# Kernel tuning notes

Hardware: AMD Instinct MI355X
Metric: run time of the kernel (lower is better)

## Reference

```python
import jax, jax.numpy as jnp
import numpy as np

P = 16; H_IMG = 384; W_IMG = 384; D = 1024
N_LAYERS = 24; DI = 2048; DS = 16; DTR = 64; DC = 4; EPS = 1e-5


def setup_inputs() -> dict:
    key = jax.random.key(0)
    ks = jax.random.split(key, 12)
    B = 2
    inp = {}
    inp["x"] = jax.random.normal(ks[0], (B, 3, H_IMG, W_IMG), jnp.float32)
    inp["patch_w"] = jax.random.normal(ks[1], (D, 3, P, P), jnp.float32) * 0.02
    inp["patch_b"] = jnp.zeros((D,), jnp.float32)
    inp["pos_embed"] = jax.random.normal(ks[2], (1, (H_IMG // P) * (W_IMG // P), D), jnp.float32) * 0.02
    inp["ln_g"] = jnp.ones((N_LAYERS, D), jnp.float32)
    inp["ln_b"] = jnp.zeros((N_LAYERS, D), jnp.float32)
    inp["in_w"] = jax.random.normal(ks[3], (N_LAYERS, 2 * DI, D), jnp.float32) * 0.02
    inp["conv_w"] = jax.random.normal(ks[4], (N_LAYERS, DI, DC), jnp.float32) * 0.1
    inp["conv_b"] = jnp.zeros((N_LAYERS, DI), jnp.float32)
    inp["xproj_w"] = jax.random.normal(ks[5], (N_LAYERS, DTR + 2 * DS, DI), jnp.float32) * 0.02
    inp["dt_w"] = jax.random.normal(ks[6], (N_LAYERS, DI, DTR), jnp.float32) * 0.02
    inp["dt_b"] = jnp.full((N_LAYERS, DI), -4.0, jnp.float32)  # softplus(-4) ~ 0.018
    inp["A_log"] = jnp.broadcast_to(jnp.log(jnp.arange(1, DS + 1, dtype=jnp.float32)), (N_LAYERS, DI, DS)).copy()
    inp["D_param"] = jnp.ones((N_LAYERS, DI), jnp.float32)
    inp["out_w"] = jax.random.normal(ks[7], (N_LAYERS, D, DI), jnp.float32) * 0.02
    return inp


def _layer_norm(x, g, b):
    mu = jnp.mean(x, axis=-1, keepdims=True)
    var = jnp.var(x, axis=-1, keepdims=True)
    return (x - mu) * jax.lax.rsqrt(var + EPS) * g + b


def _mamba_block(x, p):
    g, bn, Win, Wc, bc, Wxp, Wdt, bdt, Alog, Dd, Wout = p
    u = _layer_norm(x, g, bn)                          # [B,L,D]
    xz = jnp.einsum('bld,ed->ble', u, Win)             # [B,L,2*DI]
    xi, z = jnp.split(xz, 2, axis=-1)
    # causal depthwise conv1d along L (kernel DC=4)
    xt = jnp.moveaxis(xi, 1, 2)                        # [B,DI,L]
    L = xt.shape[-1]
    xpad = jnp.pad(xt, ((0, 0), (0, 0), (DC - 1, 0)))
    xc = sum(Wc[:, k][None, :, None] * xpad[:, :, k:k + L] for k in range(DC)) + bc[None, :, None]
    xc = jax.nn.silu(jnp.moveaxis(xc, 1, 2))           # [B,L,DI]
    dbc = jnp.einsum('bld,ed->ble', xc, Wxp)           # [B,L,DTR+2*DS]
    dt, Bm, Cm = jnp.split(dbc, [DTR, DTR + DS], axis=-1)
    dt = jax.nn.softplus(jnp.einsum('blr,dr->bld', dt, Wdt) + bdt)  # [B,L,DI]
    A = -jnp.exp(Alog)                                 # [DI,DS]
    dA = jnp.exp(dt[..., None] * A)                    # [B,L,DI,DS]
    dBx = (dt * xc)[..., None] * Bm[:, :, None, :]     # [B,L,DI,DS]

    def step(h, inp):
        dA_t, dBx_t, C_t = inp
        h = dA_t * h + dBx_t                           # [B,DI,DS]
        y = jnp.einsum('bds,bs->bd', h, C_t)
        return h, y

    h0 = jnp.zeros((x.shape[0], DI, DS), x.dtype)
    xs = (jnp.moveaxis(dA, 1, 0), jnp.moveaxis(dBx, 1, 0), jnp.moveaxis(Cm, 1, 0))
    _, ys = jax.lax.scan(step, h0, xs)                 # ys: [L,B,DI]
    y = jnp.moveaxis(ys, 0, 1) + Dd * xc
    y = y * jax.nn.silu(z)
    return x + jnp.einsum('ble,de->bld', y, Wout)


def _forward(x, patch_w, patch_b, pos_embed, ln_g, ln_b, in_w, conv_w, conv_b,
             xproj_w, dt_w, dt_b, A_log, D_param, out_w):
    feat = jax.lax.conv_general_dilated(
        x, patch_w, (P, P), 'VALID',
        dimension_numbers=('NCHW', 'OIHW', 'NCHW')) + patch_b[None, :, None, None]
    Bn, Dd, Hh, Ww = feat.shape
    tok = feat.reshape(Bn, Dd, Hh * Ww).transpose(0, 2, 1)  # [B,L,D]
    h0, w0 = H_IMG // P, W_IMG // P
    pe = pos_embed.reshape(1, h0, w0, Dd)
    pe = jax.image.resize(pe, (1, Hh, Ww, Dd), 'bilinear')  # align_corners=False
    tok = tok + pe.reshape(1, Hh * Ww, Dd)
    params = (ln_g, ln_b, in_w, conv_w, conv_b, xproj_w, dt_w, dt_b, A_log, D_param, out_w)

    def layer(carry, p):
        return jax.checkpoint(_mamba_block)(carry, p), None

    tok, _ = jax.lax.scan(layer, tok, params)
    return tok


def reference(x, patch_w, patch_b, pos_embed, ln_g, ln_b, in_w, conv_w, conv_b,
              xproj_w, dt_w, dt_b, A_log, D_param, out_w):
    return _forward(x, patch_w, patch_b, pos_embed, ln_g, ln_b, in_w, conv_w, conv_b,
                    xproj_w, dt_w, dt_b, A_log, D_param, out_w)
```

## Files before the change

### kernel.cpp

```cpp
#include <hip/hip_runtime.h>
#include <hip/hip_bf16.h>
#include <math.h>

#define PATCH   16
#define HIMG    384
#define WIMG    384
#define DMODEL  1024
#define NLAYERS 24
#define DI      2048
#define DSTATE  16
#define DTR     64
#define DC      4
#define LN_EPS  1e-5f
#define BATCH   2
#define GRIDTOK 24
#define LTOK    (GRIDTOK*GRIDTOK)
#define NTOK    (BATCH*LTOK)
#define KPATCH  (3*PATCH*PATCH)
#define NCH     16
#define LC      (LTOK/NCH)

typedef __attribute__((ext_vector_type(8))) short short8;
typedef __attribute__((ext_vector_type(4))) float f32x4;

__device__ __forceinline__ float sigmoidf_(float v) { return 1.f / (1.f + __expf(-v)); }
__device__ __forceinline__ unsigned short f2bf(float f) {
    __hip_bfloat16 h = __float2bfloat16(f);
    return *(unsigned short*)&h;
}

__global__ void im2col_kernel(const float* __restrict__ x, float* __restrict__ xcol) {
    int idx = blockIdx.x * blockDim.x + threadIdx.x;
    if (idx >= NTOK * KPATCH) return;
    int t = idx / KPATCH, k = idx % KPATCH;
    int b = t / LTOK, hw = t % LTOK;
    int h = hw / GRIDTOK, w = hw % GRIDTOK;
    int c = k / (PATCH*PATCH), r = k % (PATCH*PATCH);
    int i = r / PATCH, j = r % PATCH;
    xcol[idx] = x[(((size_t)(b*3 + c)*HIMG) + h*PATCH + i)*WIMG + w*PATCH + j];
}

__global__ __launch_bounds__(256) void layernorm_kernel(
        const float* __restrict__ x, const float* __restrict__ g,
        const float* __restrict__ b, unsigned short* __restrict__ u) {
    const int t = blockIdx.x;
    const int tid = threadIdx.x;
    const float4 xv = ((const float4*)(x + (size_t)t * DMODEL))[tid];
    float s = xv.x + xv.y + xv.z + xv.w;
    float q = xv.x*xv.x + xv.y*xv.y + xv.z*xv.z + xv.w*xv.w;
    #pragma unroll
    for (int off = 32; off >= 1; off >>= 1) {
        s += __shfl_xor(s, off);
        q += __shfl_xor(q, off);
    }
    __shared__ float red[8];
    if ((tid & 63) == 0) { red[tid >> 6] = s; red[4 + (tid >> 6)] = q; }
    __syncthreads();
    s = red[0] + red[1] + red[2] + red[3];
    q = red[4] + red[5] + red[6] + red[7];
    const float mu   = s * (1.f / DMODEL);
    const float var  = q * (1.f / DMODEL) - mu * mu;
    const float rstd = rsqrtf(var + LN_EPS);
    const float4 gv = ((const float4*)g)[tid];
    const float4 bv = ((const float4*)b)[tid];
    ushort4 o;
    o.x = f2bf((xv.x - mu) * rstd * gv.x + bv.x);
    o.y = f2bf((xv.y - mu) * rstd * gv.y + bv.y);
    o.z = f2bf((xv.z - mu) * rstd * gv.z + bv.z);
    o.w = f2bf((xv.w - mu) * rstd * gv.w + bv.w);
    ((ushort4*)(u + (size_t)t * DMODEL))[tid] = o;
}

template<int SPLITK>
__global__ __launch_bounds__(256) void gemm_mfma_bt(
        const unsigned short* __restrict__ A, int lda,
        const float* __restrict__ B, int ldb,
        float* __restrict__ C, int M, int N, int Ksub) {
    __shared__ unsigned short As[128 * 64];
    __shared__ unsigned short Bs[128 * 64];
    const int tid = threadIdx.x;
    const int m0 = blockIdx.x * 128;
    const int n0 = blockIdx.y * 128;
    const int koff = SPLITK ? blockIdx.z * Ksub : 0;
    if (SPLITK) C += (size_t)blockIdx.z * M * N;

    const int lane = tid & 63;
    const int wid  = tid >> 6;
    const int wm = (wid >> 1) * 64;
    const int wn = (wid & 1) * 64;
    const int fr = lane & 15;
    const int cb = lane >> 4;

    const int srow = tid >> 3;
    const int skc  = tid & 7;

    f32x4 acc[4][4];
    #pragma unroll
    for (int i = 0; i < 4; ++i)
        #pragma unroll
        for (int j = 0; j < 4; ++j) acc[i][j] = (f32x4){0.f, 0.f, 0.f, 0.f};

    uint4  areg[4];
    float4 breg[4][2];

    const int nk = Ksub / 64;
    #pragma unroll
    for (int i = 0; i < 4; ++i) {
        const int r = srow + 32 * i;
        areg[i] = *(const uint4*)(A + (size_t)(m0 + r) * lda + koff + skc * 8);
        const float* bp = B + (size_t)(n0 + r) * ldb + koff + skc * 8;
        breg[i][0] = *(const float4*)bp;
        breg[i][1] = *(const float4*)(bp + 4);
    }

    for (int ks = 0; ks < nk; ++ks) {
        __syncthreads();
        #pragma unroll
        for (int i = 0; i < 4; ++i) {
            const int r = srow + 32 * i;
            const int idx = r * 64 + ((skc ^ (r & 7)) << 3);
            *(uint4*)&As[idx] = areg[i];
            const float* bf = (const float*)&breg[i][0];
            short8 hv;
            #pragma unroll
            for (int j = 0; j < 8; ++j) hv[j] = (short)f2bf(bf[j]);
            *(short8*)&Bs[idx] = hv;
        }
        __syncthreads();
        if (ks + 1 < nk) {
            const int k1 = koff + (ks + 1) * 64;
            #pragma unroll
            for (int i = 0; i < 4; ++i) {
                const int r = srow + 32 * i;
                areg[i] = *(const uint4*)(A + (size_t)(m0 + r) * lda + k1 + skc * 8);
                const float* bp = B + (size_t)(n0 + r) * ldb + k1 + skc * 8;
                breg[i][0] = *(const float4*)bp;
                breg[i][1] = *(const float4*)(bp + 4);
            }
        }
        #pragma unroll
        for (int kk = 0; kk < 2; ++kk) {
            short8 af[4], bfr[4];
            #pragma unroll
            for (int mi = 0; mi < 4; ++mi) {
                const int row = wm + mi * 16 + fr;
                af[mi] = *(const short8*)&As[row * 64 + (((kk * 4 + cb) ^ (row & 7)) << 3)];
            }
            #pragma unroll
            for (int ni = 0; ni < 4; ++ni) {
                const int row = wn + ni * 16 + fr;
                bfr[ni] = *(const short8*)&Bs[row * 64 + (((kk * 4 + cb) ^ (row & 7)) << 3)];
            }
            #pragma unroll
            for (int mi = 0; mi < 4; ++mi)
                #pragma unroll
                for (int ni = 0; ni < 4; ++ni)
                    acc[mi][ni] = __builtin_amdgcn_mfma_f32_16x16x32_bf16(
                        af[mi], bfr[ni], acc[mi][ni], 0, 0, 0);
        }
    }

    #pragma unroll
    for (int mi = 0; mi < 4; ++mi) {
        const int rbase = m0 + wm + mi * 16 + cb * 4;
        #pragma unroll
        for (int ni = 0; ni < 4; ++ni) {
            const int col = n0 + wn + ni * 16 + fr;
            #pragma unroll
            for (int j = 0; j < 4; ++j)
                C[(size_t)(rbase + j) * N + col] = acc[mi][ni][j];
        }
    }
}

__global__ void reduce4_resadd_kernel(const float* __restrict__ part,
                                      float* __restrict__ tok, int n4) {
    int i = blockIdx.x * blockDim.x + threadIdx.x;
    if (i >= n4) return;
    float4 v = ((const float4*)part)[i];
    const float4 p1 = ((const float4*)part)[(size_t)1 * n4 + i];
    const float4 p2 = ((const float4*)part)[(size_t)2 * n4 + i];
    const float4 p3 = ((const float4*)part)[(size_t)3 * n4 + i];
    float4 t = ((float4*)tok)[i];
    t.x += v.x + p1.x + p2.x + p3.x;
    t.y += v.y + p1.y + p2.y + p3.y;
    t.z += v.z + p1.z + p2.z + p3.z;
    t.w += v.w + p1.w + p2.w + p3.w;
    ((float4*)tok)[i] = t;
}

enum { E_NONE = 0, E_BIAS_POS = 1, E_BIAS_SOFTPLUS = 2 };

template<int EPI>
__global__ __launch_bounds__(256) void gemm_nt(
        const float* __restrict__ A, int lda,
        const float* __restrict__ B, int ldb,
        float* __restrict__ C, int M, int N, int Ksub,
        const float* __restrict__ bias, const float* __restrict__ aux) {
    __shared__ float As[16][64];
    __shared__ float Bs[16][64];
    const int tid = threadIdx.x;
    const int m0 = blockIdx.x * 64;
    const int n0 = blockIdx.y * 64;
    const int koff = blockIdx.z * Ksub;
    C += (size_t)blockIdx.z * M * N;

    const int lrow = tid >> 2;
    const int kq   = tid & 3;
    const float* aptr = A + (size_t)(m0 + lrow) * lda + koff + kq * 4;
    const bool   bok  = (n0 + lrow) < N;
    const float* bptr = B + (size_t)(n0 + lrow) * ldb + koff + kq * 4;

    float acc[4][4] = {{0.f}};
    for (int k0 = 0; k0 < Ksub; k0 += 16) {
        const float4 av = *(const float4*)(aptr + k0);
        const float4 bv = bok ? *(const float4*)(bptr + k0) : make_float4(0.f, 0.f, 0.f, 0.f);
        __syncthreads();
        As[kq*4+0][lrow] = av.x; As[kq*4+1][lrow] = av.y;
        As[kq*4+2][lrow] = av.z; As[kq*4+3][lrow] = av.w;
        Bs[kq*4+0][lrow] = bv.x; Bs[kq*4+1][lrow] = bv.y;
        Bs[kq*4+2][lrow] = bv.z; Bs[kq*4+3][lrow] = bv.w;
        __syncthreads();
        #pragma unroll
        for (int kk = 0; kk < 16; ++kk) {
            const float4 a = *(const float4*)&As[kk][(tid >> 4) << 2];
            const float4 b = *(const float4*)&Bs[kk][(tid & 15) << 2];
            const float aa[4] = {a.x, a.y, a.z, a.w};
            const float bb[4] = {b.x, b.y, b.z, b.w};
            #pragma unroll
            for (int i = 0; i < 4; ++i)
                #pragma unroll
                for (int j = 0; j < 4; ++j)
                    acc[i][j] = fmaf(aa[i], bb[j], acc[i][j]);
        }
    }

    const int mb = m0 + ((tid >> 4) << 2);
    const int nb = n0 + ((tid & 15) << 2);
    if (nb >= N) return;
    #pragma unroll
    for (int i = 0; i < 4; ++i) {
        const int m = mb + i;
        float4 v = make_float4(acc[i][0], acc[i][1], acc[i][2], acc[i][3]);
        float* cp = C + (size_t)m * N + nb;
        if (EPI == E_BIAS_POS) {
            const float4 bz = *(const float4*)(bias + nb);
            const float4 pz = *(const float4*)(aux + (size_t)(m % LTOK) * DMODEL + nb);
            v.x += bz.x + pz.x; v.y += bz.y + pz.y; v.z += bz.z + pz.z; v.w += bz.w + pz.w;
        } else if (EPI == E_BIAS_SOFTPLUS) {
            const float4 bz = *(const float4*)(bias + nb);
            v.x += bz.x; v.y += bz.y; v.z += bz.z; v.w += bz.w;
            v.x = (v.x > 20.f) ? v.x : log1pf(__expf(v.x));
            v.y = (v.y > 20.f) ? v.y : log1pf(__expf(v.y));
            v.z = (v.z > 20.f) ? v.z : log1pf(__expf(v.z));
            v.w = (v.w > 20.f) ? v.w : log1pf(__expf(v.w));
        }
        *(float4*)cp = v;
    }
}

__global__ void conv1d_silu_kernel(const float* __restrict__ xz,
                                   const float* __restrict__ wc,
                                   const float* __restrict__ bc,
                                   float* __restrict__ xc) {
    int idx = blockIdx.x * blockDim.x + threadIdx.x;
    if (idx >= NTOK * DI) return;
    const int t = idx >> 11;
    const int e = idx & (DI - 1);
    const int l = t % LTOK;
    const float4 w = *(const float4*)(wc + e * DC);
    const float* xp = xz + (size_t)t * (2*DI) + e;
    float acc = bc[e] + w.w * xp[0];
    if (l >= 1) acc += w.z * xp[-(2*DI)];
    if (l >= 2) acc += w.y * xp[-2*(2*DI)];
    if (l >= 3) acc += w.x * xp[-3*(2*DI)];
    xc[idx] = acc * sigmoidf_(acc);
}

__global__ __launch_bounds__(256) void scan_pass1(
        const float* __restrict__ dt, const float* __restrict__ xc,
        const float* __restrict__ dbc, const float* __restrict__ Alog,
        float* __restrict__ Fst, float* __restrict__ sdt) {
    const int tid = threadIdx.x;
    const int e  = blockIdx.x * 256 + tid;
    const int c  = blockIdx.y;
    const int b  = blockIdx.z;
    const int l0 = c * LC;
    const size_t tb = (size_t)b * LTOK + l0;

    __shared__ float Bs[LC][16];
    for (int idx = tid; idx < LC * 16; idx += 256) {
        const int row = idx >> 4, s = idx & 15;
        Bs[row][s] = dbc[(tb + row) * 96 + 64 + s];
    }

    float Aval[DSTATE];
    {
        const float* ap = Alog + (size_t)e * DSTATE;
        #pragma unroll
        for (int s = 0; s < DSTATE; ++s) Aval[s] = -__expf(ap[s]);
    }
    __syncthreads();

    const float* dtp = dt + tb * DI + e;
    const float* xcp = xc + tb * DI + e;
    float h[DSTATE];
    #pragma unroll
    for (int s = 0; s < DSTATE; ++s) h[s] = 0.f;
    float sum_dt = 0.f;

    float dtv = dtp[0], xcv = xcp[0];
    for (int l = 0; l < LC; ++l) {
        float dtn = 0.f, xcn = 0.f;
        if (l + 1 < LC) { dtn = dtp[(size_t)(l+1) * DI]; xcn = xcp[(size_t)(l+1) * DI]; }
        sum_dt += dtv;
        const float dx = dtv * xcv;
        const float4* brow = (const float4*)&Bs[l][0];
        const float4 b0 = brow[0], b1 = brow[1], b2 = brow[2], b3 = brow[3];
        const float bb[16] = {b0.x,b0.y,b0.z,b0.w, b1.x,b1.y,b1.z,b1.w,
                              b2.x,b2.y,b2.z,b2.w, b3.x,b3.y,b3.z,b3.w};
        #pragma unroll
        for (int s = 0; s < DSTATE; ++s)
            h[s] = fmaf(__expf(dtv * Aval[s]), h[s], dx * bb[s]);
        dtv = dtn; xcv = xcn;
    }

    float4* Fp = (float4*)(Fst + ((((size_t)b * NCH + c) * DI) + e) * DSTATE);
    #pragma unroll
    for (int q = 0; q < 4; ++q)
        Fp[q] = make_float4(h[q*4+0], h[q*4+1], h[q*4+2], h[q*4+3]);
    sdt[((size_t)b * NCH + c) * DI + e] = sum_dt;
}

__global__ __launch_bounds__(256) void scan_pass2(
        const float* __restrict__ Fst, const float* __restrict__ sdt,
        const float* __restrict__ Alog, float* __restrict__ Hst) {
    const int idx = blockIdx.x * 256 + threadIdx.x;
    const int s = idx & 15;
    const int e = (idx >> 4) & (DI - 1);
    const int b = idx >> 15;
    const float Aval = -__expf(Alog[(size_t)e * DSTATE + s]);
    float h = 0.f;
    for (int c = 0; c < NCH; ++c) {
        const size_t base = ((size_t)b * NCH + c) * DI + e;
        Hst[base * DSTATE + s] = h;
        h = fmaf(__expf(Aval * sdt[base]), h, Fst[base * DSTATE + s]);
    }
}

__global__ __launch_bounds__(256) void scan_pass3(
        const float* __restrict__ dt, const float* __restrict__ xc,
        const float* __restrict__ dbc, const float* __restrict__ xz,
        const float* __restrict__ Alog, const float* __restrict__ Dp,
        const float* __restrict__ Hst, unsigned short* __restrict__ y) {
    const int tid = threadIdx.x;
    const int e  = blockIdx.x * 256 + tid;
    const int c  = blockIdx.y;
    const int b  = blockIdx.z;
    const int l0 = c * LC;
    const size_t tb = (size_t)b * LTOK + l0;

    __shared__ float BCs[LC][32];
    for (int idx = tid; idx < LC * 32; idx += 256) {
        const int row = idx >> 5, col = idx & 31;
        BCs[row][col] = dbc[(tb + row) * 96 + 64 + col];
    }

    float Aval[DSTATE];
    {
        const float* ap = Alog + (size_t)e * DSTATE;
        #pragma unroll
        for (int s = 0; s < DSTATE; ++s) Aval[s] = -__expf(ap[s]);
    }
    const float Dv = Dp[e];

    float h[DSTATE];
    {
        const float4* Hp = (const float4*)(Hst + ((((size_t)b * NCH + c) * DI) + e) * DSTATE);
        #pragma unroll
        for (int q = 0; q < 4; ++q) {
            const float4 hv = Hp[q];
            h[q*4+0] = hv.x; h[q*4+1] = hv.y; h[q*4+2] = hv.z; h[q*4+3] = hv.w;
        }
    }
    __syncthreads();

    const float* dtp = dt + tb * DI + e;
    const float* xcp = xc + tb * DI + e;
    const float* zp  = xz + tb * (2*DI) + DI + e;
    unsigned short* yp = y + tb * DI + e;

    float dtv = dtp[0], xcv = xcp[0], zv = zp[0];
    for (int l = 0; l < LC; ++l) {
        float dtn = 0.f, xcn = 0.f, zn = 0.f;
        if (l + 1 < LC) {
            dtn = dtp[(size_t)(l+1) * DI];
            xcn = xcp[(size_t)(l+1) * DI];
            zn  = zp[(size_t)(l+1) * (2*DI)];
        }
        const float dx = dtv * xcv;
        const float4* brow = (const float4*)&BCs[l][0];
        const float4 b0 = brow[0], b1 = brow[1], b2 = brow[2], b3 = brow[3];
        const float4 c0 = brow[4], c1 = brow[5], c2 = brow[6], c3 = brow[7];
        const float bb[16] = {b0.x,b0.y,b0.z,b0.w, b1.x,b1.y,b1.z,b1.w,
                              b2.x,b2.y,b2.z,b2.w, b3.x,b3.y,b3.z,b3.w};
        const float cc[16] = {c0.x,c0.y,c0.z,c0.w, c1.x,c1.y,c1.z,c1.w,
                              c2.x,c2.y,c2.z,c2.w, c3.x,c3.y,c3.z,c3.w};
        float yv = 0.f;
        #pragma unroll
        for (int s = 0; s < DSTATE; ++s) {
            h[s] = fmaf(__expf(dtv * Aval[s]), h[s], dx * bb[s]);
            yv = fmaf(h[s], cc[s], yv);
        }
        yp[(size_t)l * DI] = f2bf((yv + Dv * xcv) * (zv * sigmoidf_(zv)));
        dtv = dtn; xcv = xcn; zv = zn;
    }
}

__global__ void reduce8_kernel(const float* __restrict__ part, float* __restrict__ out, int n) {
    int i = blockIdx.x * blockDim.x + threadIdx.x;
    if (i >= n) return;
    float s = 0.f;
    #pragma unroll
    for (int z = 0; z < 8; ++z) s += part[(size_t)z * n + i];
    out[i] = s;
}

extern "C" void kernel_launch(void* const* d_in, const int* in_sizes, int n_in,
                              void* d_out, int out_size, void* d_ws, size_t ws_size,
                              hipStream_t stream) {
    const float* x       = (const float*)d_in[0];
    const float* patch_w = (const float*)d_in[1];
    const float* patch_b = (const float*)d_in[2];
    const float* pos     = (const float*)d_in[3];
    const float* ln_g    = (const float*)d_in[4];
    const float* ln_b    = (const float*)d_in[5];
    const float* in_w    = (const float*)d_in[6];
    const float* conv_w  = (const float*)d_in[7];
    const float* conv_b  = (const float*)d_in[8];
    const float* xproj_w = (const float*)d_in[9];
    const float* dt_w    = (const float*)d_in[10];
    const float* dt_b    = (const float*)d_in[11];
    const float* A_log   = (const float*)d_in[12];
    const float* D_par   = (const float*)d_in[13];
    const float* out_w   = (const float*)d_in[14];

    float* tok = (float*)d_out;
    float* ws  = (float*)d_ws;
    float* Xcol = ws;  ws += (size_t)NTOK * KPATCH;
    unsigned short* u_bf = (unsigned short*)ws; ws += (size_t)NTOK * DMODEL / 2;
    float* xz   = ws;  ws += (size_t)NTOK * 2 * DI;
    float* xc   = ws;  ws += (size_t)NTOK * DI;
    float* dbcP = ws;  ws += (size_t)8 * NTOK * 96;
    float* dbc  = ws;  ws += (size_t)NTOK * 96;
    float* dtb  = ws;  ws += (size_t)NTOK * DI;
    unsigned short* yb_bf = (unsigned short*)ws; ws += (size_t)NTOK * DI / 2;
    float* Fst  = ws;  ws += (size_t)BATCH * NCH * DI * DSTATE;
    float* Hst  = ws;  ws += (size_t)BATCH * NCH * DI * DSTATE;
    float* sdt  = ws;  ws += (size_t)BATCH * NCH * DI;

    im2col_kernel<<<(NTOK*KPATCH + 255)/256, 256, 0, stream>>>(x, Xcol);
    gemm_nt<E_BIAS_POS><<<dim3(NTOK/64, DMODEL/64), 256, 0, stream>>>(
        Xcol, KPATCH, patch_w, KPATCH, tok, NTOK, DMODEL, KPATCH, patch_b, pos);

    for (int layer = 0; layer < NLAYERS; ++layer) {
        const float* Wg  = ln_g    + (size_t)layer * DMODEL;
        const float* Wb  = ln_b    + (size_t)layer * DMODEL;
        const float* Win = in_w    + (size_t)layer * 2 * DI * DMODEL;
        const float* Wc  = conv_w  + (size_t)layer * DI * DC;
        const float* Bc  = conv_b  + (size_t)layer * DI;
        const float* Wxp = xproj_w + (size_t)layer * 96 * DI;
        const float* Wdt = dt_w    + (size_t)layer * DI * DTR;
        const float* Bdt = dt_b    + (size_t)layer * DI;
        const float* Al  = A_log   + (size_t)layer * DI * DSTATE;
        const float* Dd  = D_par   + (size_t)layer * DI;
        const float* Wo  = out_w   + (size_t)layer * DMODEL * DI;

        layernorm_kernel<<<NTOK, 256, 0, stream>>>(tok, Wg, Wb, u_bf);
        gemm_mfma_bt<0><<<dim3(NTOK/128, (2*DI)/128, 1), 256, 0, stream>>>(
            u_bf, DMODEL, Win, DMODEL, xz, NTOK, 2*DI, DMODEL);
        conv1d_silu_kernel<<<(NTOK*DI + 255)/256, 256, 0, stream>>>(xz, Wc, Bc, xc);
        gemm_nt<E_NONE><<<dim3(NTOK/64, 2, 8), 256, 0, stream>>>(
            xc, DI, Wxp, DI, dbcP, NTOK, 96, DI/8, nullptr, nullptr);
        reduce8_kernel<<<(NTOK*96 + 255)/256, 256, 0, stream>>>(dbcP, dbc, NTOK*96);
        gemm_nt<E_BIAS_SOFTPLUS><<<dim3(NTOK/64, DI/64), 256, 0, stream>>>(
            dbc, 96, Wdt, DTR, dtb, NTOK, DI, DTR, Bdt, nullptr);
        scan_pass1<<<dim3(DI/256, NCH, BATCH), 256, 0, stream>>>(
            dtb, xc, dbc, Al, Fst, sdt);
        scan_pass2<<<(BATCH*DI*DSTATE)/256, 256, 0, stream>>>(Fst, sdt, Al, Hst);
        scan_pass3<<<dim3(DI/256, NCH, BATCH), 256, 0, stream>>>(
            dtb, xc, dbc, xz, Al, Dd, Hst, yb_bf);
        gemm_mfma_bt<1><<<dim3(NTOK/128, DMODEL/128, 4), 256, 0, stream>>>(
            yb_bf, DI, Wo, DI, xz, NTOK, DMODEL, DI/4);
        reduce4_resadd_kernel<<<(NTOK*DMODEL/4 + 255)/256, 256, 0, stream>>>(
            xz, tok, NTOK*DMODEL/4);
    }
}
```

Measured before the change: 4.660 ms.

## Pre-convert weights to bf16, move small GEMMs to MFMA, fuse reduce with layernorm

Every weight matrix is converted to bf16 once at the start, so the MFMA GEMMs load bf16 B tiles directly instead of converting fp32 inside the inner loop. The patch embedding, x-projection and dt-projection GEMMs move from scalar fp32 FMA kernels to bf16 MFMA kernels, with a dedicated 96-column kernel for x-proj. The split-K residual reduce is fused with the next layer's layernorm. scan_pass2 is removed by having pass3 recompute the chunk prefix state itself. The weight conversion pass adds extra memory traffic per call, and the bf16 inputs to the small projections lower precision.

```diff
diff --git a/kernel.cpp b/kernel.cpp
--- a/kernel.cpp
+++ b/kernel.cpp
@@ -29,7 +29,16 @@
     return *(unsigned short*)&h;
 }
 
-__global__ void im2col_kernel(const float* __restrict__ x, float* __restrict__ xcol) {
+__global__ void f2bf_kernel(const float* __restrict__ in, unsigned short* __restrict__ out, int n4) {
+    for (int i = blockIdx.x * blockDim.x + threadIdx.x; i < n4; i += gridDim.x * blockDim.x) {
+        const float4 v = ((const float4*)in)[i];
+        ushort4 o;
+        o.x = f2bf(v.x); o.y = f2bf(v.y); o.z = f2bf(v.z); o.w = f2bf(v.w);
+        ((ushort4*)out)[i] = o;
+    }
+}
+
+__global__ void im2col_kernel(const float* __restrict__ x, unsigned short* __restrict__ xcol) {
     int idx = blockIdx.x * blockDim.x + threadIdx.x;
     if (idx >= NTOK * KPATCH) return;
     int t = idx / KPATCH, k = idx % KPATCH;
@@ -37,7 +46,7 @@
     int h = hw / GRIDTOK, w = hw % GRIDTOK;
     int c = k / (PATCH*PATCH), r = k % (PATCH*PATCH);
     int i = r / PATCH, j = r % PATCH;
-    xcol[idx] = x[(((size_t)(b*3 + c)*HIMG) + h*PATCH + i)*WIMG + w*PATCH + j];
+    xcol[idx] = f2bf(x[(((size_t)(b*3 + c)*HIMG) + h*PATCH + i)*WIMG + w*PATCH + j]);
 }
 
 __global__ __launch_bounds__(256) void layernorm_kernel(
@@ -71,11 +80,12 @@
     ((ushort4*)(u + (size_t)t * DMODEL))[tid] = o;
 }
 
-template<int SPLITK>
-__global__ __launch_bounds__(256) void gemm_mfma_bt(
+template<int SPLITK, int EPI>
+__global__ __launch_bounds__(256) void gemm_bb(
         const unsigned short* __restrict__ A, int lda,
-        const float* __restrict__ B, int ldb,
-        float* __restrict__ C, int M, int N, int Ksub) {
+        const unsigned short* __restrict__ B, int ldb,
+        float* __restrict__ C, int M, int N, int Ksub,
+        const float* __restrict__ bias, const float* __restrict__ aux) {
     __shared__ unsigned short As[128 * 64];
     __shared__ unsigned short Bs[128 * 64];
     const int tid = threadIdx.x;
@@ -100,17 +110,13 @@
         #pragma unroll
         for (int j = 0; j < 4; ++j) acc[i][j] = (f32x4){0.f, 0.f, 0.f, 0.f};
 
-    uint4  areg[4];
-    float4 breg[4][2];
-
+    uint4 areg[4], breg[4];
     const int nk = Ksub / 64;
     #pragma unroll
     for (int i = 0; i < 4; ++i) {
         const int r = srow + 32 * i;
         areg[i] = *(const uint4*)(A + (size_t)(m0 + r) * lda + koff + skc * 8);
-        const float* bp = B + (size_t)(n0 + r) * ldb + koff + skc * 8;
-        breg[i][0] = *(const float4*)bp;
-        breg[i][1] = *(const float4*)(bp + 4);
+        breg[i] = *(const uint4*)(B + (size_t)(n0 + r) * ldb + koff + skc * 8);
     }
 
     for (int ks = 0; ks < nk; ++ks) {
@@ -120,11 +126,7 @@
             const int r = srow + 32 * i;
             const int idx = r * 64 + ((skc ^ (r & 7)) << 3);
             *(uint4*)&As[idx] = areg[i];
-            const float* bf = (const float*)&breg[i][0];
-            short8 hv;
-            #pragma unroll
-            for (int j = 0; j < 8; ++j) hv[j] = (short)f2bf(bf[j]);
-            *(short8*)&Bs[idx] = hv;
+            *(uint4*)&Bs[idx] = breg[i];
         }
         __syncthreads();
         if (ks + 1 < nk) {
@@ -133,9 +135,7 @@
             for (int i = 0; i < 4; ++i) {
                 const int r = srow + 32 * i;
                 areg[i] = *(const uint4*)(A + (size_t)(m0 + r) * lda + k1 + skc * 8);
-                const float* bp = B + (size_t)(n0 + r) * ldb + k1 + skc * 8;
-                breg[i][0] = *(const float4*)bp;
-                breg[i][1] = *(const float4*)(bp + 4);
+                breg[i] = *(const uint4*)(B + (size_t)(n0 + r) * ldb + k1 + skc * 8);
             }
         }
         #pragma unroll
@@ -167,102 +167,133 @@
         for (int ni = 0; ni < 4; ++ni) {
             const int col = n0 + wn + ni * 16 + fr;
             #pragma unroll
+            for (int j = 0; j < 4; ++j) {
+                float v = acc[mi][ni][j];
+                if (EPI == 1) {
+                    v += bias[col];
+                    v = (v > 20.f) ? v : log1pf(__expf(v));
+                } else if (EPI == 2) {
+                    v += bias[col] + aux[(size_t)((rbase + j) % LTOK) * DMODEL + col];
+                }
+                C[(size_t)(rbase + j) * N + col] = v;
+            }
+        }
+    }
+}
+
+__global__ __launch_bounds__(256) void gemm_xproj(
+        const unsigned short* __restrict__ A,
+        const unsigned short* __restrict__ B,
+        float* __restrict__ C) {
+    __shared__ unsigned short As[128 * 64];
+    __shared__ unsigned short Bs[96 * 64];
+    const int tid = threadIdx.x;
+    const int m0 = blockIdx.x * 128;
+    const int koff = blockIdx.y * (DI / 8);
+    C += (size_t)blockIdx.y * NTOK * 96;
+
+    const int lane = tid & 63;
+    const int wid  = tid >> 6;
+    const int wm = wid * 32;
+    const int fr = lane & 15;
+    const int cb = lane >> 4;
+    const int srow = tid >> 3;
+    const int skc  = tid & 7;
+
+    f32x4 acc[2][6];
+    #pragma unroll
+    for (int i = 0; i < 2; ++i)
+        #pragma unroll
+        for (int j = 0; j < 6; ++j) acc[i][j] = (f32x4){0.f, 0.f, 0.f, 0.f};
+
+    uint4 areg[4], breg[3];
+    #pragma unroll
+    for (int i = 0; i < 4; ++i)
+        areg[i] = *(const uint4*)(A + (size_t)(m0 + srow + 32 * i) * DI + koff + skc * 8);
+    #pragma unroll
+    for (int i = 0; i < 3; ++i) {
+        const int idx = tid + 256 * i;
+        breg[i] = *(const uint4*)(B + (size_t)(idx >> 3) * DI + koff + (idx & 7) * 8);
+    }
+
+    const int nk = (DI / 8) / 64;
+    for (int ks = 0; ks < nk; ++ks) {
+        __syncthreads();
+        #pragma unroll
+        for (int i = 0; i < 4; ++i) {
+            const int r = srow + 32 * i;
+            *(uint4*)&As[r * 64 + ((skc ^ (r & 7)) << 3)] = areg[i];
+        }
+        #pragma unroll
+        for (int i = 0; i < 3; ++i) {
+            const int idx = tid + 256 * i;
+            const int r = idx >> 3, kc = idx & 7;
+            *(uint4*)&Bs[r * 64 + ((kc ^ (r & 7)) << 3)] = breg[i];
+        }
+        __syncthreads();
+        if (ks + 1 < nk) {
+            const int k1 = koff + (ks + 1) * 64;
+            #pragma unroll
+            for (int i = 0; i < 4; ++i)
+                areg[i] = *(const uint4*)(A + (size_t)(m0 + srow + 32 * i) * DI + k1 + skc * 8);
+            #pragma unroll
+            for (int i = 0; i < 3; ++i) {
+                const int idx = tid + 256 * i;
+                breg[i] = *(const uint4*)(B + (size_t)(idx >> 3) * DI + k1 + (idx & 7) * 8);
+            }
+        }
+        #pragma unroll
+        for (int kk = 0; kk < 2; ++kk) {
+            short8 af[2], bfr[6];
+            #pragma unroll
+            for (int mi = 0; mi < 2; ++mi) {
+                const int row = wm + mi * 16 + fr;
+                af[mi] = *(const short8*)&As[row * 64 + (((kk * 4 + cb) ^ (row & 7)) << 3)];
+            }
+            #pragma unroll
+            for (int ni = 0; ni < 6; ++ni) {
+                const int row = ni * 16 + fr;
+                bfr[ni] = *(const short8*)&Bs[row * 64 + (((kk * 4 + cb) ^ (row & 7)) << 3)];
+            }
+            #pragma unroll
+            for (int mi = 0; mi < 2; ++mi)
+                #pragma unroll
+                for (int ni = 0; ni < 6; ++ni)
+                    acc[mi][ni] = __builtin_amdgcn_mfma_f32_16x16x32_bf16(
+                        af[mi], bfr[ni], acc[mi][ni], 0, 0, 0);
+        }
+    }
+
+    #pragma unroll
+    for (int mi = 0; mi < 2; ++mi) {
+        const int rbase = m0 + wm + mi * 16 + cb * 4;
+        #pragma unroll
+        for (int ni = 0; ni < 6; ++ni) {
+            const int col = ni * 16 + fr;
+            #pragma unroll
             for (int j = 0; j < 4; ++j)
-                C[(size_t)(rbase + j) * N + col] = acc[mi][ni][j];
-        }
-    }
-}
-
-__global__ void reduce4_resadd_kernel(const float* __restrict__ part,
-                                      float* __restrict__ tok, int n4) {
+                C[(size_t)(rbase + j) * 96 + col] = acc[mi][ni][j];
+        }
+    }
+}
+
+__global__ void reduce8_kernel(const float* __restrict__ part, float* __restrict__ out,
+                               unsigned short* __restrict__ out64, int n) {
     int i = blockIdx.x * blockDim.x + threadIdx.x;
-    if (i >= n4) return;
-    float4 v = ((const float4*)part)[i];
-    const float4 p1 = ((const float4*)part)[(size_t)1 * n4 + i];
-    const float4 p2 = ((const float4*)part)[(size_t)2 * n4 + i];
-    const float4 p3 = ((const float4*)part)[(size_t)3 * n4 + i];
-    float4 t = ((float4*)tok)[i];
-    t.x += v.x + p1.x + p2.x + p3.x;
-    t.y += v.y + p1.y + p2.y + p3.y;
-    t.z += v.z + p1.z + p2.z + p3.z;
-    t.w += v.w + p1.w + p2.w + p3.w;
-    ((float4*)tok)[i] = t;
-}
-
-enum { E_NONE = 0, E_BIAS_POS = 1, E_BIAS_SOFTPLUS = 2 };
-
-template<int EPI>
-__global__ __launch_bounds__(256) void gemm_nt(
-        const float* __restrict__ A, int lda,
-        const float* __restrict__ B, int ldb,
-        float* __restrict__ C, int M, int N, int Ksub,
-        const float* __restrict__ bias, const float* __restrict__ aux) {
-    __shared__ float As[16][64];
-    __shared__ float Bs[16][64];
-    const int tid = threadIdx.x;
-    const int m0 = blockIdx.x * 64;
-    const int n0 = blockIdx.y * 64;
-    const int koff = blockIdx.z * Ksub;
-    C += (size_t)blockIdx.z * M * N;
-
-    const int lrow = tid >> 2;
-    const int kq   = tid & 3;
-    const float* aptr = A + (size_t)(m0 + lrow) * lda + koff + kq * 4;
-    const bool   bok  = (n0 + lrow) < N;
-    const float* bptr = B + (size_t)(n0 + lrow) * ldb + koff + kq * 4;
-
-    float acc[4][4] = {{0.f}};
-    for (int k0 = 0; k0 < Ksub; k0 += 16) {
-        const float4 av = *(const float4*)(aptr + k0);
-        const float4 bv = bok ? *(const float4*)(bptr + k0) : make_float4(0.f, 0.f, 0.f, 0.f);
-        __syncthreads();
-        As[kq*4+0][lrow] = av.x; As[kq*4+1][lrow] = av.y;
-        As[kq*4+2][lrow] = av.z; As[kq*4+3][lrow] = av.w;
-        Bs[kq*4+0][lrow] = bv.x; Bs[kq*4+1][lrow] = bv.y;
-        Bs[kq*4+2][lrow] = bv.z; Bs[kq*4+3][lrow] = bv.w;
-        __syncthreads();
-        #pragma unroll
-        for (int kk = 0; kk < 16; ++kk) {
-            const float4 a = *(const float4*)&As[kk][(tid >> 4) << 2];
-            const float4 b = *(const float4*)&Bs[kk][(tid & 15) << 2];
-            const float aa[4] = {a.x, a.y, a.z, a.w};
-            const float bb[4] = {b.x, b.y, b.z, b.w};
-            #pragma unroll
-            for (int i = 0; i < 4; ++i)
-                #pragma unroll
-                for (int j = 0; j < 4; ++j)
-                    acc[i][j] = fmaf(aa[i], bb[j], acc[i][j]);
-        }
-    }
-
-    const int mb = m0 + ((tid >> 4) << 2);
-    const int nb = n0 + ((tid & 15) << 2);
-    if (nb >= N) return;
-    #pragma unroll
-    for (int i = 0; i < 4; ++i) {
-        const int m = mb + i;
-        float4 v = make_float4(acc[i][0], acc[i][1], acc[i][2], acc[i][3]);
-        float* cp = C + (size_t)m * N + nb;
-        if (EPI == E_BIAS_POS) {
-            const float4 bz = *(const float4*)(bias + nb);
-            const float4 pz = *(const float4*)(aux + (size_t)(m % LTOK) * DMODEL + nb);
-            v.x += bz.x + pz.x; v.y += bz.y + pz.y; v.z += bz.z + pz.z; v.w += bz.w + pz.w;
-        } else if (EPI == E_BIAS_SOFTPLUS) {
-            const float4 bz = *(const float4*)(bias + nb);
-            v.x += bz.x; v.y += bz.y; v.z += bz.z; v.w += bz.w;
-            v.x = (v.x > 20.f) ? v.x : log1pf(__expf(v.x));
-            v.y = (v.y > 20.f) ? v.y : log1pf(__expf(v.y));
-            v.z = (v.z > 20.f) ? v.z : log1pf(__expf(v.z));
-            v.w = (v.w > 20.f) ? v.w : log1pf(__expf(v.w));
-        }
-        *(float4*)cp = v;
-    }
+    if (i >= n) return;
+    float s = 0.f;
+    #pragma unroll
+    for (int z = 0; z < 8; ++z) s += part[(size_t)z * n + i];
+    out[i] = s;
+    const int col = i % 96;
+    if (col < 64) out64[(i / 96) * 64 + col] = f2bf(s);
 }
 
 __global__ void conv1d_silu_kernel(const float* __restrict__ xz,
                                    const float* __restrict__ wc,
                                    const float* __restrict__ bc,
-                                   float* __restrict__ xc) {
+                                   float* __restrict__ xc,
+                                   unsigned short* __restrict__ xc_bf) {
     int idx = blockIdx.x * blockDim.x + threadIdx.x;
     if (idx >= NTOK * DI) return;
     const int t = idx >> 11;
@@ -274,7 +305,9 @@
     if (l >= 1) acc += w.z * xp[-(2*DI)];
     if (l >= 2) acc += w.y * xp[-2*(2*DI)];
     if (l >= 3) acc += w.x * xp[-3*(2*DI)];
-    xc[idx] = acc * sigmoidf_(acc);
+    const float r = acc * sigmoidf_(acc);
+    xc[idx] = r;
+    xc_bf[idx] = f2bf(r);
 }
 
 __global__ __launch_bounds__(256) void scan_pass1(
@@ -332,27 +365,12 @@
     sdt[((size_t)b * NCH + c) * DI + e] = sum_dt;
 }
 
-__global__ __launch_bounds__(256) void scan_pass2(
-        const float* __restrict__ Fst, const float* __restrict__ sdt,
-        const float* __restrict__ Alog, float* __restrict__ Hst) {
-    const int idx = blockIdx.x * 256 + threadIdx.x;
-    const int s = idx & 15;
-    const int e = (idx >> 4) & (DI - 1);
-    const int b = idx >> 15;
-    const float Aval = -__expf(Alog[(size_t)e * DSTATE + s]);
-    float h = 0.f;
-    for (int c = 0; c < NCH; ++c) {
-        const size_t base = ((size_t)b * NCH + c) * DI + e;
-        Hst[base * DSTATE + s] = h;
-        h = fmaf(__expf(Aval * sdt[base]), h, Fst[base * DSTATE + s]);
-    }
-}
-
 __global__ __launch_bounds__(256) void scan_pass3(
         const float* __restrict__ dt, const float* __restrict__ xc,
         const float* __restrict__ dbc, const float* __restrict__ xz,
         const float* __restrict__ Alog, const float* __restrict__ Dp,
-        const float* __restrict__ Hst, unsigned short* __restrict__ y) {
+        const float* __restrict__ Fst, const float* __restrict__ sdt,
+        unsigned short* __restrict__ y) {
     const int tid = threadIdx.x;
     const int e  = blockIdx.x * 256 + tid;
     const int c  = blockIdx.y;
@@ -375,13 +393,18 @@
     const float Dv = Dp[e];
 
     float h[DSTATE];
-    {
-        const float4* Hp = (const float4*)(Hst + ((((size_t)b * NCH + c) * DI) + e) * DSTATE);
-        #pragma unroll
-        for (int q = 0; q < 4; ++q) {
-            const float4 hv = Hp[q];
-            h[q*4+0] = hv.x; h[q*4+1] = hv.y; h[q*4+2] = hv.z; h[q*4+3] = hv.w;
-        }
+    #pragma unroll
+    for (int s = 0; s < DSTATE; ++s) h[s] = 0.f;
+    for (int c2 = 0; c2 < c; ++c2) {
+        const size_t base = ((size_t)b * NCH + c2) * DI + e;
+        const float sd = sdt[base];
+        const float4* Fp = (const float4*)(Fst + base * DSTATE);
+        const float4 f0 = Fp[0], f1 = Fp[1], f2 = Fp[2], f3 = Fp[3];
+        const float ff[16] = {f0.x,f0.y,f0.z,f0.w, f1.x,f1.y,f1.z,f1.w,
+                              f2.x,f2.y,f2.z,f2.w, f3.x,f3.y,f3.z,f3.w};
+        #pragma unroll
+        for (int s = 0; s < DSTATE; ++s)
+            h[s] = fmaf(__expf(Aval[s] * sd), h[s], ff[s]);
     }
     __syncthreads();
 
@@ -417,13 +440,50 @@
     }
 }
 
-__global__ void reduce8_kernel(const float* __restrict__ part, float* __restrict__ out, int n) {
-    int i = blockIdx.x * blockDim.x + threadIdx.x;
-    if (i >= n) return;
-    float s = 0.f;
-    #pragma unroll
-    for (int z = 0; z < 8; ++z) s += part[(size_t)z * n + i];
-    out[i] = s;
+template<bool DO_LN>
+__global__ __launch_bounds__(256) void reduce4_ln_kernel(
+        const float* __restrict__ part, float* __restrict__ tok,
+        const float* __restrict__ g, const float* __restrict__ b,
+        unsigned short* __restrict__ u) {
+    const int t = blockIdx.x;
+    const int tid = threadIdx.x;
+    const int n4 = NTOK * DMODEL / 4;
+    const int i = t * 256 + tid;
+    float4 v = ((const float4*)part)[i];
+    const float4 p1 = ((const float4*)part)[(size_t)1 * n4 + i];
+    const float4 p2 = ((const float4*)part)[(size_t)2 * n4 + i];
+    const float4 p3 = ((const float4*)part)[(size_t)3 * n4 + i];
+    float4 tv = ((float4*)tok)[i];
+    tv.x += v.x + p1.x + p2.x + p3.x;
+    tv.y += v.y + p1.y + p2.y + p3.y;
+    tv.z += v.z + p1.z + p2.z + p3.z;
+    tv.w += v.w + p1.w + p2.w + p3.w;
+    ((float4*)tok)[i] = tv;
+    if (DO_LN) {
+        float s = tv.x + tv.y + tv.z + tv.w;
+        float q = tv.x*tv.x + tv.y*tv.y + tv.z*tv.z + tv.w*tv.w;
+        #pragma unroll
+        for (int off = 32; off >= 1; off >>= 1) {
+            s += __shfl_xor(s, off);
+            q += __shfl_xor(q, off);
+        }
+        __shared__ float red[8];
+        if ((tid & 63) == 0) { red[tid >> 6] = s; red[4 + (tid >> 6)] = q; }
+        __syncthreads();
+        s = red[0] + red[1] + red[2] + red[3];
+        q = red[4] + red[5] + red[6] + red[7];
+        const float mu   = s * (1.f / DMODEL);
+        const float var  = q * (1.f / DMODEL) - mu * mu;
+        const float rstd = rsqrtf(var + LN_EPS);
+        const float4 gv = ((const float4*)g)[tid];
+        const float4 bv = ((const float4*)b)[tid];
+        ushort4 o;
+        o.x = f2bf((tv.x - mu) * rstd * gv.x + bv.x);
+        o.y = f2bf((tv.y - mu) * rstd * gv.y + bv.y);
+        o.z = f2bf((tv.z - mu) * rstd * gv.z + bv.z);
+        o.w = f2bf((tv.w - mu) * rstd * gv.w + bv.w);
+        ((ushort4*)(u + (size_t)t * DMODEL))[tid] = o;
+    }
 }
 
 extern "C" void kernel_launch(void* const* d_in, const int* in_sizes, int n_in,
@@ -447,52 +507,66 @@
 
     float* tok = (float*)d_out;
     float* ws  = (float*)d_ws;
-    float* Xcol = ws;  ws += (size_t)NTOK * KPATCH;
-    unsigned short* u_bf = (unsigned short*)ws; ws += (size_t)NTOK * DMODEL / 2;
     float* xz   = ws;  ws += (size_t)NTOK * 2 * DI;
     float* xc   = ws;  ws += (size_t)NTOK * DI;
     float* dbcP = ws;  ws += (size_t)8 * NTOK * 96;
     float* dbc  = ws;  ws += (size_t)NTOK * 96;
     float* dtb  = ws;  ws += (size_t)NTOK * DI;
-    unsigned short* yb_bf = (unsigned short*)ws; ws += (size_t)NTOK * DI / 2;
     float* Fst  = ws;  ws += (size_t)BATCH * NCH * DI * DSTATE;
-    float* Hst  = ws;  ws += (size_t)BATCH * NCH * DI * DSTATE;
     float* sdt  = ws;  ws += (size_t)BATCH * NCH * DI;
-
-    im2col_kernel<<<(NTOK*KPATCH + 255)/256, 256, 0, stream>>>(x, Xcol);
-    gemm_nt<E_BIAS_POS><<<dim3(NTOK/64, DMODEL/64), 256, 0, stream>>>(
-        Xcol, KPATCH, patch_w, KPATCH, tok, NTOK, DMODEL, KPATCH, patch_b, pos);
+    unsigned short* us = (unsigned short*)ws;
+    unsigned short* Xcol_bf  = us; us += (size_t)NTOK * KPATCH;
+    unsigned short* u_bf     = us; us += (size_t)NTOK * DMODEL;
+    unsigned short* xc_bf    = us; us += (size_t)NTOK * DI;
+    unsigned short* yb_bf    = us; us += (size_t)NTOK * DI;
+    unsigned short* dbc64_bf = us; us += (size_t)NTOK * 64;
+    unsigned short* winb  = us; us += (size_t)NLAYERS * 2 * DI * DMODEL;
+    unsigned short* woutb = us; us += (size_t)NLAYERS * DMODEL * DI;
+    unsigned short* wxpb  = us; us += (size_t)NLAYERS * 96 * DI;
+    unsigned short* wdtb  = us; us += (size_t)NLAYERS * DI * DTR;
+    unsigned short* wpb   = us; us += (size_t)DMODEL * KPATCH;
+
+    f2bf_kernel<<<2048, 256, 0, stream>>>(in_w,    winb,  NLAYERS*2*DI*DMODEL/4);
+    f2bf_kernel<<<2048, 256, 0, stream>>>(out_w,   woutb, NLAYERS*DMODEL*DI/4);
+    f2bf_kernel<<<1024, 256, 0, stream>>>(xproj_w, wxpb,  NLAYERS*96*DI/4);
+    f2bf_kernel<<<1024, 256, 0, stream>>>(dt_w,    wdtb,  NLAYERS*DI*DTR/4);
+    f2bf_kernel<<<256,  256, 0, stream>>>(patch_w, wpb,   DMODEL*KPATCH/4);
+
+    im2col_kernel<<<(NTOK*KPATCH + 255)/256, 256, 0, stream>>>(x, Xcol_bf);
+    gemm_bb<0, 2><<<dim3(NTOK/128, DMODEL/128), 256, 0, stream>>>(
+        Xcol_bf, KPATCH, wpb, KPATCH, tok, NTOK, DMODEL, KPATCH, patch_b, pos);
+
+    layernorm_kernel<<<NTOK, 256, 0, stream>>>(tok, ln_g, ln_b, u_bf);
 
     for (int layer = 0; layer < NLAYERS; ++layer) {
-        const float* Wg  = ln_g    + (size_t)layer * DMODEL;
-        const float* Wb  = ln_b    + (size_t)layer * DMODEL;
-        const float* Win = in_w    + (size_t)layer * 2 * DI * DMODEL;
-        const float* Wc  = conv_w  + (size_t)layer * DI * DC;
-        const float* Bc  = conv_b  + (size_t)layer * DI;
-        const float* Wxp = xproj_w + (size_t)layer * 96 * DI;
-        const float* Wdt = dt_w    + (size_t)layer * DI * DTR;
-        const float* Bdt = dt_b    + (size_t)layer * DI;
-        const float* Al  = A_log   + (size_t)layer * DI * DSTATE;
-        const float* Dd  = D_par   + (size_t)layer * DI;
-        const float* Wo  = out_w   + (size_t)layer * DMODEL * DI;
-
-        layernorm_kernel<<<NTOK, 256, 0, stream>>>(tok, Wg, Wb, u_bf);
-        gemm_mfma_bt<0><<<dim3(NTOK/128, (2*DI)/128, 1), 256, 0, stream>>>(
-            u_bf, DMODEL, Win, DMODEL, xz, NTOK, 2*DI, DMODEL);
-        conv1d_silu_kernel<<<(NTOK*DI + 255)/256, 256, 0, stream>>>(xz, Wc, Bc, xc);
-        gemm_nt<E_NONE><<<dim3(NTOK/64, 2, 8), 256, 0, stream>>>(
-            xc, DI, Wxp, DI, dbcP, NTOK, 96, DI/8, nullptr, nullptr);
-        reduce8_kernel<<<(NTOK*96 + 255)/256, 256, 0, stream>>>(dbcP, dbc, NTOK*96);
-        gemm_nt<E_BIAS_SOFTPLUS><<<dim3(NTOK/64, DI/64), 256, 0, stream>>>(
-            dbc, 96, Wdt, DTR, dtb, NTOK, DI, DTR, Bdt, nullptr);
+        const unsigned short* Win = winb  + (size_t)layer * 2 * DI * DMODEL;
+        const unsigned short* Wo  = woutb + (size_t)layer * DMODEL * DI;
+        const unsigned short* Wxp = wxpb  + (size_t)layer * 96 * DI;
+        const unsigned short* Wdt = wdtb  + (size_t)layer * DI * DTR;
+        const float* Wc  = conv_w + (size_t)layer * DI * DC;
+        const float* Bc  = conv_b + (size_t)layer * DI;
+        const float* Bdt = dt_b   + (size_t)layer * DI;
+        const float* Al  = A_log  + (size_t)layer * DI * DSTATE;
+        const float* Dd  = D_par  + (size_t)layer * DI;
+
+        gemm_bb<0, 0><<<dim3(NTOK/128, (2*DI)/128), 256, 0, stream>>>(
+            u_bf, DMODEL, Win, DMODEL, xz, NTOK, 2*DI, DMODEL, nullptr, nullptr);
+        conv1d_silu_kernel<<<(NTOK*DI + 255)/256, 256, 0, stream>>>(xz, Wc, Bc, xc, xc_bf);
+        gemm_xproj<<<dim3(NTOK/128, 8), 256, 0, stream>>>(xc_bf, Wxp, dbcP);
+        reduce8_kernel<<<(NTOK*96 + 255)/256, 256, 0, stream>>>(dbcP, dbc, dbc64_bf, NTOK*96);
+        gemm_bb<0, 1><<<dim3(NTOK/128, DI/128), 256, 0, stream>>>(
+            dbc64_bf, 64, Wdt, DTR, dtb, NTOK, DI, DTR, Bdt, nullptr);
         scan_pass1<<<dim3(DI/256, NCH, BATCH), 256, 0, stream>>>(
             dtb, xc, dbc, Al, Fst, sdt);
-        scan_pass2<<<(BATCH*DI*DSTATE)/256, 256, 0, stream>>>(Fst, sdt, Al, Hst);
         scan_pass3<<<dim3(DI/256, NCH, BATCH), 256, 0, stream>>>(
-            dtb, xc, dbc, xz, Al, Dd, Hst, yb_bf);
-        gemm_mfma_bt<1><<<dim3(NTOK/128, DMODEL/128, 4), 256, 0, stream>>>(
-            yb_bf, DI, Wo, DI, xz, NTOK, DMODEL, DI/4);
-        reduce4_resadd_kernel<<<(NTOK*DMODEL/4 + 255)/256, 256, 0, stream>>>(
-            xz, tok, NTOK*DMODEL/4);
-    }
-}
+            dtb, xc, dbc, xz, Al, Dd, Fst, sdt, yb_bf);
+        gemm_bb<1, 0><<<dim3(NTOK/128, DMODEL/128, 4), 256, 0, stream>>>(
+            yb_bf, DI, Wo, DI, xz, NTOK, DMODEL, DI/4, nullptr, nullptr);
+        if (layer < NLAYERS - 1)
+            reduce4_ln_kernel<true><<<NTOK, 256, 0, stream>>>(
+                xz, tok, ln_g + (size_t)(layer+1) * DMODEL, ln_b + (size_t)(layer+1) * DMODEL, u_bf);
+        else
+            reduce4_ln_kernel<false><<<NTOK, 256, 0, stream>>>(
+                xz, tok, nullptr, nullptr, u_bf);
+    }
+}
```

After: 6.178 ms. 32.6% more time.
